# Optimization experiments

Measured on AMD Instinct MI355X. Metric: run time of the kernel, lower is better.

Reference implementation:

```python
import jax, jax.numpy as jnp
import numpy as np

EMBED = 1024
HEADS = 16
HEAD_DIM = EMBED // HEADS          # 64
POS_DIM = 256
POS_PER_HEAD = POS_DIM // HEADS    # 16
POS_IDX = 64
N, L = 8, 1024


def setup_inputs() -> dict:
    key = jax.random.key(0)
    ks = jax.random.split(key, 10)
    s = 0.02
    return {
        "values": jax.random.normal(ks[0], (N, L, EMBED), jnp.float32),
        "keys": jax.random.normal(ks[1], (N, L, EMBED), jnp.float32),
        "query": jax.random.normal(ks[2], (N, L, EMBED), jnp.float32),
        "position": jax.random.normal(ks[3], (N, L, POS_IDX), jnp.float32),
        # torch Linear weights: shape (out_features, in_features)
        "Wv": jax.random.normal(ks[4], (HEAD_DIM, HEAD_DIM), jnp.float32) * s,
        "Wk": jax.random.normal(ks[5], (HEAD_DIM, HEAD_DIM), jnp.float32) * s,
        "Wq": jax.random.normal(ks[6], (HEAD_DIM, HEAD_DIM + POS_PER_HEAD), jnp.float32) * s,
        "Wpos": jax.random.normal(ks[7], (POS_DIM, POS_IDX), jnp.float32) * s,
        "Wo": jax.random.normal(ks[8], (EMBED, EMBED), jnp.float32) * s,
        "bo": jax.random.normal(ks[9], (EMBED,), jnp.float32) * s,
    }


def reference(values, keys, query, position, Wv, Wk, Wq, Wpos, Wo, bo):
    n, qlen = query.shape[0], query.shape[1]
    vlen, klen = values.shape[1], keys.shape[1]
    # position embedding: Linear(pos_idx -> pos_dim)
    pos_emb = position @ Wpos.T                                   # [N, q, POS_DIM]
    q_with_pos = jnp.concatenate([query, pos_emb], axis=2)        # [N, q, EMBED+POS_DIM]
    # split heads
    v = values.reshape(n, vlen, HEADS, HEAD_DIM)
    k = keys.reshape(n, klen, HEADS, HEAD_DIM)
    qp = q_with_pos.reshape(n, qlen, HEADS, HEAD_DIM + POS_PER_HEAD)
    # per-head linear projections (no bias)
    v = jnp.einsum('nlhd,ed->nlhe', v, Wv)
    k = jnp.einsum('nlhd,ed->nlhe', k, Wk)
    q = jnp.einsum('nqhd,ed->nqhe', qp, Wq)
    # attention: note scale uses sqrt(embed_size), as in the original
    energy = jnp.einsum('nqhd,nkhd->nhqk', q, k)
    attn = jax.nn.softmax(energy / jnp.sqrt(jnp.asarray(EMBED, energy.dtype)), axis=3)
    out = jnp.einsum('nhql,nlhd->nqhd', attn, v).reshape(n, qlen, EMBED)
    return out @ Wo.T + bo
```

## Files before the change

### kernel.cpp

```cpp
#include <hip/hip_runtime.h>
#include <hip/hip_bf16.h>


typedef __hip_bfloat16 bf16;
typedef unsigned int u32;
typedef unsigned short u16;
typedef short short8 __attribute__((ext_vector_type(8)));
typedef float f32x4 __attribute__((ext_vector_type(4)));
typedef float f32x16 __attribute__((ext_vector_type(16)));
typedef unsigned int u32x2 __attribute__((ext_vector_type(2)));

#define MFMA16(a, b, c) __builtin_amdgcn_mfma_f32_16x16x32_bf16((a), (b), (c), 0, 0, 0)
#define MFMA32(a, b, c) __builtin_amdgcn_mfma_f32_32x32x16_bf16((a), (b), (c), 0, 0, 0)

#define QSCALE 0.04508422002777998f

__device__ __forceinline__ short8 ld8(const bf16* p) { return *(const short8*)p; }

__device__ __forceinline__ u32 pk2(float a, float b) {
  u16 ua = __bfloat16_as_ushort(__float2bfloat16(a));
  u16 ub = __bfloat16_as_ushort(__float2bfloat16(b));
  return (u32)ua | ((u32)ub << 16);
}

__device__ __forceinline__ float fexp2(float x) {
  float r;
  asm("v_exp_f32 %0, %1" : "=v"(r) : "v"(x));
  return r;
}

__device__ __forceinline__ u32 cvtpk(float a, float b) {
  u32 r;
  asm("v_cvt_pk_bf16_f32 %0, %1, %2" : "=v"(r) : "v"(a), "v"(b));
  return r;
}

__device__ __forceinline__ void gload16(const void* g, void* l) {
  __builtin_amdgcn_global_load_lds(
      (const __attribute__((address_space(1))) u32*)g,
      (__attribute__((address_space(3))) u32*)l, 16, 0, 0);
}

union S8U { short8 s; u32 u[4]; };

__device__ __forceinline__ short8 ld8f(const float* p) {
  float4 a = ((const float4*)p)[0];
  float4 b = ((const float4*)p)[1];
  S8U r;
  r.u[0] = pk2(a.x, a.y);
  r.u[1] = pk2(a.z, a.w);
  r.u[2] = pk2(b.x, b.y);
  r.u[3] = pk2(b.z, b.w);
  return r.s;
}

__global__ __launch_bounds__(256) void fused_pre(
    const float* __restrict__ position, const float* __restrict__ Wpos,
    const float* __restrict__ keys, const float* __restrict__ Wk,
    const float* __restrict__ values, const float* __restrict__ Wv,
    const float* __restrict__ Wo,
    bf16* __restrict__ posb, bf16* __restrict__ kb, bf16* __restrict__ vT,
    bf16* __restrict__ wo16) {
  __shared__ __align__(16) char arena[33280];
  const int bidg = blockIdx.x;
  const int t = threadIdx.x;
  const int lane = t & 63, wave = t >> 6;
  const int g = lane >> 4, c = lane & 15;
  const int wr = wave >> 1, wc = wave & 1;

  if (bidg < 128) {
    const int px = bidg & 63, py = bidg >> 6;
    const int r0 = px * 128 + wr * 64;
    const int c0 = py * 128 + wc * 64;
    f32x4 acc[4][4];
#pragma unroll
    for (int ai = 0; ai < 4; ++ai)
#pragma unroll
      for (int bi = 0; bi < 4; ++bi) acc[ai][bi] = (f32x4){0.f, 0.f, 0.f, 0.f};
#pragma unroll
    for (int k0 = 0; k0 < 64; k0 += 32) {
      short8 af[4], bfr[4];
#pragma unroll
      for (int ai = 0; ai < 4; ++ai)
        af[ai] = ld8f(position + (size_t)(r0 + ai * 16 + c) * 64 + k0 + 8 * g);
#pragma unroll
      for (int bi = 0; bi < 4; ++bi)
        bfr[bi] = ld8f(Wpos + (size_t)(c0 + bi * 16 + c) * 64 + k0 + 8 * g);
#pragma unroll
      for (int ai = 0; ai < 4; ++ai)
#pragma unroll
        for (int bi = 0; bi < 4; ++bi) acc[ai][bi] = MFMA16(af[ai], bfr[bi], acc[ai][bi]);
    }
#pragma unroll
    for (int bi = 0; bi < 4; ++bi) {
      const int p = c0 + bi * 16 + c;
#pragma unroll
      for (int ai = 0; ai < 4; ++ai) {
#pragma unroll
        for (int i = 0; i < 4; ++i) {
          int row = r0 + ai * 16 + 4 * g + i;
          posb[(size_t)row * 256 + p] = __float2bfloat16(acc[ai][bi][i]);
        }
      }
    }
  } else if (bidg < 2176) {
    const bool is_v = (bidg >= 1152);
    const int id = bidg - (is_v ? 1152 : 128);
    const int bx = id & 63, h = id >> 6;
    const float* src = is_v ? values : keys;
    const float* W = is_v ? Wv : Wk;
    f32x4 acc[4][2];
#pragma unroll
    for (int ai = 0; ai < 4; ++ai)
#pragma unroll
      for (int bi = 0; bi < 2; ++bi) acc[ai][bi] = (f32x4){0.f, 0.f, 0.f, 0.f};
    const int r0 = bx * 128;
    const int c0 = wc * 32;
#pragma unroll
    for (int k0 = 0; k0 < 64; k0 += 32) {
      short8 af[4], bfr[2];
#pragma unroll
      for (int ai = 0; ai < 4; ++ai)
        af[ai] = ld8f(src + (size_t)(r0 + wr * 64 + ai * 16 + c) * 1024 + 64 * h + k0 + 8 * g);
#pragma unroll
      for (int bi = 0; bi < 2; ++bi)
        bfr[bi] = ld8f(W + (size_t)(c0 + bi * 16 + c) * 64 + k0 + 8 * g);
#pragma unroll
      for (int ai = 0; ai < 4; ++ai)
#pragma unroll
        for (int bi = 0; bi < 2; ++bi) acc[ai][bi] = MFMA16(af[ai], bfr[bi], acc[ai][bi]);
    }
    if (!is_v) {
      float (*slds)[65] = (float(*)[65])arena;
#pragma unroll
      for (int bi = 0; bi < 2; ++bi) {
        const int e = c0 + bi * 16 + c;
#pragma unroll
        for (int ai = 0; ai < 4; ++ai) {
#pragma unroll
          for (int i = 0; i < 4; ++i)
            slds[wr * 64 + ai * 16 + 4 * g + i][e] = acc[ai][bi][i];
        }
      }
      __syncthreads();
      const int n = r0 >> 10, lb = r0 & 1023;
      bf16* dstp = kb + ((size_t)(n * 16 + h) * 1024 + lb) * 64;
#pragma unroll
      for (int j = 0; j < 4; ++j) {
        const int id2 = t + j * 256;
        const int ll = id2 >> 3, e0 = (id2 & 7) * 8;
        const float* s = &slds[ll][e0];
        S8U r;
        r.u[0] = pk2(s[0], s[1]);
        r.u[1] = pk2(s[2], s[3]);
        r.u[2] = pk2(s[4], s[5]);
        r.u[3] = pk2(s[6], s[7]);
        *(short8*)(dstp + (size_t)ll * 64 + e0) = r.s;
      }
    } else {
      char* tlds = arena;
#pragma unroll
      for (int bi = 0; bi < 2; ++bi) {
        const int e_loc = c0 + bi * 16 + c;
#pragma unroll
        for (int ai = 0; ai < 4; ++ai) {
          const int l0 = wr * 64 + ai * 16 + 4 * g;
          *(u32*)(tlds + e_loc * 272 + l0 * 2) = pk2(acc[ai][bi][0], acc[ai][bi][1]);
          *(u32*)(tlds + e_loc * 272 + l0 * 2 + 4) = pk2(acc[ai][bi][2], acc[ai][bi][3]);
        }
      }
      __syncthreads();
      const int n = bx >> 3;
      const int lglob0 = (bx & 7) * 128;
      bf16* vbase = vT + ((size_t)(n * 16 + h)) * 64 * 1024;
#pragma unroll
      for (int j = 0; j < 4; ++j) {
        const int id2 = t + j * 256;
        const int e = id2 >> 4, lc = (id2 & 15) * 8;
        *(short8*)(vbase + (size_t)e * 1024 + lglob0 + lc) =
            *(const short8*)(tlds + e * 272 + lc * 2);
      }
    }
  } else {
    const int id = bidg - 2176;
    const int i8 = (id * 256 + t) * 8;
    *(short8*)(wo16 + i8) = ld8f(Wo + i8);
  }
}

__global__ __launch_bounds__(256) void q_gemm(const float* __restrict__ query,
                                              const bf16* __restrict__ posb,
                                              const float* __restrict__ Wq,
                                              bf16* __restrict__ qb) {
  __shared__ float slds[128][65];
  const int t = threadIdx.x;
  const int lane = t & 63, wave = t >> 6;
  const int g = lane >> 4, c = lane & 15;
  const int wr = wave >> 1, wc = wave & 1;
  const int r0 = blockIdx.x * 128;
  const int c0 = wc * 32;
  const int h = blockIdx.y;
  f32x4 acc[4][2];
#pragma unroll
  for (int ai = 0; ai < 4; ++ai)
#pragma unroll
    for (int bi = 0; bi < 2; ++bi) acc[ai][bi] = (f32x4){0.f, 0.f, 0.f, 0.f};
  const short8 z8 = (short8){0, 0, 0, 0, 0, 0, 0, 0};
#pragma unroll
  for (int k0 = 0; k0 < 80; k0 += 32) {
    const bool tail_dead = (k0 == 64) && (g >= 2);
    const int col = 80 * h + k0 + 8 * g;
    short8 af[4], bfr[2];
#pragma unroll
    for (int ai = 0; ai < 4; ++ai) {
      const int row = r0 + wr * 64 + ai * 16 + c;
      af[ai] = tail_dead ? z8
               : (col < 1024 ? ld8f(query + (size_t)row * 1024 + col)
                             : ld8(posb + (size_t)row * 256 + (col - 1024)));
    }
#pragma unroll
    for (int bi = 0; bi < 2; ++bi)
      bfr[bi] = tail_dead ? z8
                          : ld8f(Wq + (size_t)(c0 + bi * 16 + c) * 80 + k0 + 8 * g);
#pragma unroll
    for (int ai = 0; ai < 4; ++ai)
#pragma unroll
      for (int bi = 0; bi < 2; ++bi) acc[ai][bi] = MFMA16(af[ai], bfr[bi], acc[ai][bi]);
  }
#pragma unroll
  for (int bi = 0; bi < 2; ++bi) {
    const int e = c0 + bi * 16 + c;
#pragma unroll
    for (int ai = 0; ai < 4; ++ai) {
#pragma unroll
      for (int i = 0; i < 4; ++i)
        slds[wr * 64 + ai * 16 + 4 * g + i][e] = acc[ai][bi][i] * QSCALE;
    }
  }
  __syncthreads();
  const int n = r0 >> 10, lb = r0 & 1023;
  bf16* dstp = qb + ((size_t)(n * 16 + h) * 1024 + lb) * 64;
#pragma unroll
  for (int j = 0; j < 4; ++j) {
    const int id = t + j * 256;
    const int ll = id >> 3, e0 = (id & 7) * 8;
    const float* s = &slds[ll][e0];
    S8U r;
    r.u[0] = pk2(s[0], s[1]);
    r.u[1] = pk2(s[2], s[3]);
    r.u[2] = pk2(s[4], s[5]);
    r.u[3] = pk2(s[6], s[7]);
    *(short8*)(dstp + (size_t)ll * 64 + e0) = r.s;
  }
}

__global__ __launch_bounds__(256, 2) void attn_kernel(const bf16* __restrict__ qb,
                                                      const bf16* __restrict__ kb,
                                                      const bf16* __restrict__ vT,
                                                      bf16* __restrict__ ob) {
  __shared__ __align__(16) char smem[2][16384];
  const int t = threadIdx.x;
  const int lane = t & 63, wave = t >> 6;
  const int l31 = lane & 31, hi = lane >> 5;
  const int bid = blockIdx.x;
  const int w = (bid & 7) * 64 + (bid >> 3);
  const int qt = w & 3, h = (w >> 2) & 15, n = w >> 6;
  const int nh = n * 16 + h;
  const int q0 = qt * 256 + wave * 64;

  const bf16* kpan = kb + (size_t)nh * 65536;
  const bf16* vpan = vT + (size_t)nh * 65536;

  const int sr8 = lane >> 3;
  const int scg = (lane & 7) ^ sr8;
  const int row0 = wave * 8 + sr8;
  const bf16* kgA = kpan + (size_t)row0 * 64 + scg * 8;
  const bf16* kgB = kpan + (size_t)(32 + row0) * 64 + scg * 8;
  const bf16* vgA = vpan + (size_t)row0 * 1024 + scg * 8;
  const bf16* vgB = vpan + (size_t)(32 + row0) * 1024 + scg * 8;
  const int ldsoff = wave * 1024;

  const bf16* qrowA = qb + ((size_t)nh * 1024 + q0 + l31) * 64 + 8 * hi;
  const bf16* qrowB = qrowA + 32 * 64;
  short8 qfA[4], qfB[4];
#pragma unroll
  for (int ds = 0; ds < 4; ++ds) {
    qfA[ds] = ld8(qrowA + ds * 16);
    qfB[ds] = ld8(qrowB + ds * 16);
  }

  f32x16 accA0, accA1, accB0, accB1;
#pragma unroll
  for (int r = 0; r < 16; ++r) {
    accA0[r] = 0.f;
    accA1[r] = 0.f;
    accB0[r] = 0.f;
    accB1[r] = 0.f;
  }
  float lA = 0.f, lB = 0.f;

  gload16(kgA, smem[0] + ldsoff);
  gload16(kgB, smem[0] + 4096 + ldsoff);
  gload16(vgA, smem[0] + 8192 + ldsoff);
  gload16(vgB, smem[0] + 12288 + ldsoff);
  __syncthreads();

  int cur = 0;
  for (int kt = 0; kt < 16; ++kt) {
    if (kt < 15) {
      char* sn = smem[cur ^ 1];
      const size_t ko = (size_t)(kt + 1) * 4096;
      const int vo = (kt + 1) * 64;
      gload16(kgA + ko, sn + ldsoff);
      gload16(kgB + ko, sn + 4096 + ldsoff);
      gload16(vgA + vo, sn + 8192 + ldsoff);
      gload16(vgB + vo, sn + 12288 + ldsoff);
    }
    const char* kt_ = smem[cur];
    const char* vt_ = smem[cur] + 8192;

#pragma unroll
    for (int s = 0; s < 2; ++s) {
      const int kr = s * 32 + l31;
      short8 kf[4], vf[2][2];
#pragma unroll
      for (int ds = 0; ds < 4; ++ds)
        kf[ds] = *(const short8*)(kt_ + kr * 128 + (((2 * ds + hi) ^ (kr & 7)) << 4));
#pragma unroll
      for (int dt = 0; dt < 2; ++dt) {
        const int vr = dt * 32 + l31;
#pragma unroll
        for (int ks = 0; ks < 2; ++ks)
          vf[dt][ks] = *(const short8*)(
              vt_ + vr * 128 + (((s * 4 + ks * 2 + hi) ^ (vr & 7)) << 4));
      }

      f32x16 srA, srB;
#pragma unroll
      for (int r = 0; r < 16; ++r) {
        srA[r] = 0.f;
        srB[r] = 0.f;
      }
      __builtin_amdgcn_s_setprio(1);
      srA = MFMA32(kf[0], qfA[0], srA);
      srA = MFMA32(kf[1], qfA[1], srA);
      srA = MFMA32(kf[2], qfA[2], srA);
      srA = MFMA32(kf[3], qfA[3], srA);
      srB = MFMA32(kf[0], qfB[0], srB);
      srB = MFMA32(kf[1], qfB[1], srB);
      srB = MFMA32(kf[2], qfB[2], srB);
      srB = MFMA32(kf[3], qfB[3], srB);
      __builtin_amdgcn_s_setprio(0);

      float pA[16], pB[16];
#pragma unroll
      for (int r = 0; r < 16; ++r) pA[r] = fexp2(srA[r]);
#pragma unroll
      for (int r = 0; r < 16; ++r) pB[r] = fexp2(srB[r]);

      u32 a01 = cvtpk(pA[0], pA[1]), a23 = cvtpk(pA[2], pA[3]);
      u32 a45 = cvtpk(pA[4], pA[5]), a67 = cvtpk(pA[6], pA[7]);
      u32 a89 = cvtpk(pA[8], pA[9]), aab = cvtpk(pA[10], pA[11]);
      u32 acd = cvtpk(pA[12], pA[13]), aef = cvtpk(pA[14], pA[15]);
      u32x2 sa0 = __builtin_amdgcn_permlane32_swap(a01, a45, false, false);
      u32x2 sa1 = __builtin_amdgcn_permlane32_swap(a23, a67, false, false);
      u32x2 sa2 = __builtin_amdgcn_permlane32_swap(a89, acd, false, false);
      u32x2 sa3 = __builtin_amdgcn_permlane32_swap(aab, aef, false, false);
      S8U pfA0, pfA1;
      pfA0.u[0] = sa0[0];
      pfA0.u[1] = sa1[0];
      pfA0.u[2] = sa0[1];
      pfA0.u[3] = sa1[1];
      pfA1.u[0] = sa2[0];
      pfA1.u[1] = sa3[0];
      pfA1.u[2] = sa2[1];
      pfA1.u[3] = sa3[1];

      u32 b01 = cvtpk(pB[0], pB[1]), b23 = cvtpk(pB[2], pB[3]);
      u32 b45 = cvtpk(pB[4], pB[5]), b67 = cvtpk(pB[6], pB[7]);
      u32 b89 = cvtpk(pB[8], pB[9]), bab = cvtpk(pB[10], pB[11]);
      u32 bcd = cvtpk(pB[12], pB[13]), bef = cvtpk(pB[14], pB[15]);
      u32x2 sb0 = __builtin_amdgcn_permlane32_swap(b01, b45, false, false);
      u32x2 sb1 = __builtin_amdgcn_permlane32_swap(b23, b67, false, false);
      u32x2 sb2 = __builtin_amdgcn_permlane32_swap(b89, bcd, false, false);
      u32x2 sb3 = __builtin_amdgcn_permlane32_swap(bab, bef, false, false);
      S8U pfB0, pfB1;
      pfB0.u[0] = sb0[0];
      pfB0.u[1] = sb1[0];
      pfB0.u[2] = sb0[1];
      pfB0.u[3] = sb1[1];
      pfB1.u[0] = sb2[0];
      pfB1.u[1] = sb3[0];
      pfB1.u[2] = sb2[1];
      pfB1.u[3] = sb3[1];

      __builtin_amdgcn_s_setprio(1);
      accA0 = MFMA32(vf[0][0], pfA0.s, accA0);
      accA0 = MFMA32(vf[0][1], pfA1.s, accA0);
      accA1 = MFMA32(vf[1][0], pfA0.s, accA1);
      accA1 = MFMA32(vf[1][1], pfA1.s, accA1);
      accB0 = MFMA32(vf[0][0], pfB0.s, accB0);
      accB0 = MFMA32(vf[0][1], pfB1.s, accB0);
      accB1 = MFMA32(vf[1][0], pfB0.s, accB1);
      accB1 = MFMA32(vf[1][1], pfB1.s, accB1);
      __builtin_amdgcn_s_setprio(0);

      float psA = ((pA[0] + pA[1]) + (pA[2] + pA[3])) +
                  ((pA[4] + pA[5]) + (pA[6] + pA[7])) +
                  ((pA[8] + pA[9]) + (pA[10] + pA[11])) +
                  ((pA[12] + pA[13]) + (pA[14] + pA[15]));
      float psB = ((pB[0] + pB[1]) + (pB[2] + pB[3])) +
                  ((pB[4] + pB[5]) + (pB[6] + pB[7])) +
                  ((pB[8] + pB[9]) + (pB[10] + pB[11])) +
                  ((pB[12] + pB[13]) + (pB[14] + pB[15]));
      psA += __shfl_xor(psA, 32);
      psB += __shfl_xor(psB, 32);
      lA += psA;
      lB += psB;
    }
    __syncthreads();
    cur ^= 1;
  }

  const float invA = 1.f / lA, invB = 1.f / lB;
  bf16* obaseA = ob + ((size_t)(n * 1024 + q0 + l31) * 16 + h) * 64;
  bf16* obaseB = obaseA + (size_t)32 * 16 * 64;
#pragma unroll
  for (int dt = 0; dt < 2; ++dt) {
#pragma unroll
    for (int rb = 0; rb < 4; ++rb) {
      const int d0 = dt * 32 + rb * 8 + 4 * hi;
      const f32x16& aA = dt ? accA1 : accA0;
      const f32x16& aB = dt ? accB1 : accB0;
      u32x2 wA, wB;
      wA[0] = pk2(aA[4 * rb + 0] * invA, aA[4 * rb + 1] * invA);
      wA[1] = pk2(aA[4 * rb + 2] * invA, aA[4 * rb + 3] * invA);
      wB[0] = pk2(aB[4 * rb + 0] * invB, aB[4 * rb + 1] * invB);
      wB[1] = pk2(aB[4 * rb + 2] * invB, aB[4 * rb + 3] * invB);
      *(u32x2*)(obaseA + d0) = wA;
      *(u32x2*)(obaseB + d0) = wB;
    }
  }
}

__global__ __launch_bounds__(256) void out_gemm(const bf16* __restrict__ A,
                                                const bf16* __restrict__ B,
                                                const float* __restrict__ bias,
                                                float* __restrict__ out) {
  __shared__ __align__(16) char smem[2][32768];
  const int t = threadIdx.x;
  const int lane = t & 63, wave = t >> 6;
  const int g = lane >> 4, c = lane & 15;
  const int wr = wave >> 1, wc = wave & 1;
  const int bid = blockIdx.x;
  const int w = (bid & 7) * 64 + (bid >> 3);
  const int r0 = (w >> 3) * 128;
  const int c0 = (w & 7) * 128;

  const int sr8 = lane >> 3;
  const int scg = (lane & 7) ^ sr8;
  const int row0 = wave * 8 + sr8;
  const bf16* ag = A + (size_t)(r0 + row0) * 1024 + scg * 8;
  const bf16* bg = B + (size_t)(c0 + row0) * 1024 + scg * 8;
  const int ldsoff = wave * 1024;

  f32x4 acc[4][4];
#pragma unroll
  for (int ai = 0; ai < 4; ++ai)
#pragma unroll
    for (int bi = 0; bi < 4; ++bi) acc[ai][bi] = (f32x4){0.f, 0.f, 0.f, 0.f};

#pragma unroll
  for (int j = 0; j < 4; ++j) {
    gload16(ag + (size_t)j * 32 * 1024, smem[0] + j * 4096 + ldsoff);
    gload16(bg + (size_t)j * 32 * 1024, smem[0] + 16384 + j * 4096 + ldsoff);
  }
  __syncthreads();

  int cur = 0;
  for (int kt = 0; kt < 16; ++kt) {
    if (kt < 15) {
      char* sn = smem[cur ^ 1];
      const int k1 = (kt + 1) * 64;
#pragma unroll
      for (int j = 0; j < 4; ++j) {
        gload16(ag + (size_t)j * 32 * 1024 + k1, sn + j * 4096 + ldsoff);
        gload16(bg + (size_t)j * 32 * 1024 + k1, sn + 16384 + j * 4096 + ldsoff);
      }
    }
    const char* sa = smem[cur];
    const char* sb = smem[cur] + 16384;

#pragma unroll
    for (int h2 = 0; h2 < 2; ++h2) {
      short8 af[4], bfr[4];
#pragma unroll
      for (int ai = 0; ai < 4; ++ai) {
        const int row = wr * 64 + ai * 16 + c;
        af[ai] = *(const short8*)(sa + row * 128 + (((h2 * 4 + g) ^ (row & 7)) << 4));
      }
#pragma unroll
      for (int bi = 0; bi < 4; ++bi) {
        const int row = wc * 64 + bi * 16 + c;
        bfr[bi] = *(const short8*)(sb + row * 128 + (((h2 * 4 + g) ^ (row & 7)) << 4));
      }
      __builtin_amdgcn_s_setprio(1);
#pragma unroll
      for (int ai = 0; ai < 4; ++ai)
#pragma unroll
        for (int bi = 0; bi < 4; ++bi) acc[ai][bi] = MFMA16(af[ai], bfr[bi], acc[ai][bi]);
      __builtin_amdgcn_s_setprio(0);
    }

    __syncthreads();
    cur ^= 1;
  }

#pragma unroll
  for (int bi = 0; bi < 4; ++bi) {
    const int e = c0 + wc * 64 + bi * 16 + c;
    const float bv = bias[e];
#pragma unroll
    for (int ai = 0; ai < 4; ++ai) {
#pragma unroll
      for (int i = 0; i < 4; ++i) {
        out[(size_t)(r0 + wr * 64 + ai * 16 + 4 * g + i) * 1024 + e] =
            acc[ai][bi][i] + bv;
      }
    }
  }
}

extern "C" void kernel_launch(void* const* d_in, const int* in_sizes, int n_in,
                              void* d_out, int out_size, void* d_ws, size_t ws_size,
                              hipStream_t stream) {
  const float* values = (const float*)d_in[0];
  const float* keys = (const float*)d_in[1];
  const float* query = (const float*)d_in[2];
  const float* position = (const float*)d_in[3];
  const float* Wv = (const float*)d_in[4];
  const float* Wk = (const float*)d_in[5];
  const float* Wq = (const float*)d_in[6];
  const float* Wpos = (const float*)d_in[7];
  const float* Wo = (const float*)d_in[8];
  const float* bo = (const float*)d_in[9];

  char* ws = (char*)d_ws;
  bf16* qb = (bf16*)(ws);
  bf16* kb = (bf16*)(ws + ((size_t)16 << 20));
  bf16* vT = (bf16*)(ws + ((size_t)32 << 20));
  bf16* posb = (bf16*)(ws + ((size_t)48 << 20));
  bf16* ob = (bf16*)(ws + ((size_t)52 << 20));
  bf16* wo16 = (bf16*)(ws + ((size_t)68 << 20));
  float* out = (float*)d_out;

  fused_pre<<<2688, 256, 0, stream>>>(position, Wpos, keys, Wk, values, Wv, Wo,
                                      posb, kb, vT, wo16);
  q_gemm<<<dim3(64, 16), 256, 0, stream>>>(query, posb, Wq, qb);
  attn_kernel<<<512, 256, 0, stream>>>(qb, kb, vT, ob);
  out_gemm<<<512, 256, 0, stream>>>(ob, wo16, bo, out);
}
```

Baseline: 113.5 us.

## Triple-buffer K/V tiles in attention kernel with single barrier per iteration

The attention kernel's K/V LDS staging moves from double to triple buffering, prefetching two tiles ahead. Explicit vmcnt waits and one raw s_barrier per iteration replace the trailing __syncthreads, which should hide more global-load latency and remove one barrier. The cost is 48KB of LDS per block instead of 32KB, which may limit occupancy under the 2-blocks-per-CU launch bound. Correctness relies on the hand-counted vmcnt(4) matching the four loads issued per stage.

```diff
diff --git a/kernel.cpp b/kernel.cpp
--- a/kernel.cpp
+++ b/kernel.cpp
@@ -258,7 +258,7 @@
                                                       const bf16* __restrict__ kb,
                                                       const bf16* __restrict__ vT,
                                                       bf16* __restrict__ ob) {
-  __shared__ __align__(16) char smem[2][16384];
+  __shared__ __align__(16) char smem[3][16384];
   const int t = threadIdx.x;
   const int lane = t & 63, wave = t >> 6;
   const int l31 = lane & 31, hi = lane >> 5;
@@ -299,23 +299,34 @@
   }
   float lA = 0.f, lB = 0.f;
 
-  gload16(kgA, smem[0] + ldsoff);
-  gload16(kgB, smem[0] + 4096 + ldsoff);
-  gload16(vgA, smem[0] + 8192 + ldsoff);
-  gload16(vgB, smem[0] + 12288 + ldsoff);
-  __syncthreads();
+#define STAGE(sb, kt)                                   \
+  do {                                                  \
+    char* s_ = (sb);                                    \
+    gload16(kgA + (size_t)(kt) * 4096, s_ + ldsoff);    \
+    gload16(kgB + (size_t)(kt) * 4096, s_ + 4096 + ldsoff); \
+    gload16(vgA + (kt) * 64, s_ + 8192 + ldsoff);       \
+    gload16(vgB + (kt) * 64, s_ + 12288 + ldsoff);      \
+  } while (0)
+
+  STAGE(smem[0], 0);
+  STAGE(smem[1], 1);
 
   int cur = 0;
   for (int kt = 0; kt < 16; ++kt) {
-    if (kt < 15) {
-      char* sn = smem[cur ^ 1];
-      const size_t ko = (size_t)(kt + 1) * 4096;
-      const int vo = (kt + 1) * 64;
-      gload16(kgA + ko, sn + ldsoff);
-      gload16(kgB + ko, sn + 4096 + ldsoff);
-      gload16(vgA + vo, sn + 8192 + ldsoff);
-      gload16(vgB + vo, sn + 12288 + ldsoff);
-    }
+    if (kt < 15)
+      asm volatile("s_waitcnt vmcnt(4) lgkmcnt(0)" ::: "memory");
+    else
+      asm volatile("s_waitcnt vmcnt(0) lgkmcnt(0)" ::: "memory");
+    __builtin_amdgcn_sched_barrier(0);
+    __builtin_amdgcn_s_barrier();
+    __builtin_amdgcn_sched_barrier(0);
+    if (kt + 2 < 16) {
+      int nb = cur + 2;
+      if (nb >= 3) nb -= 3;
+      STAGE(smem[nb], kt + 2);
+    }
+    __builtin_amdgcn_sched_barrier(0);
+
     const char* kt_ = smem[cur];
     const char* vt_ = smem[cur] + 8192;
 
@@ -418,9 +429,9 @@
       lA += psA;
       lB += psB;
     }
-    __syncthreads();
-    cur ^= 1;
-  }
+    cur = (cur == 2) ? 0 : cur + 1;
+  }
+#undef STAGE
 
   const float invA = 1.f / lA, invB = 1.f / lB;
   bf16* obaseA = ob + ((size_t)(n * 1024 + q0 + l31) * 16 + h) * 64;
```

After: 114.4 us. Within noise of the previous version (+0.8%).

## Move position-independent Q projection heads into the fused pre-processing kernel

Applied to the files above, without the earlier changes.

Q-projection blocks for heads 0-11 read only query columns, so they do not depend on the position embedding. They are moved into the first fused kernel as extra blocks. The remaining heads 12-15, which need posb, run in a smaller follow-up kernel. This shrinks the serialized second launch and lets the independent Q work overlap with the K/V/pos conversion, at the cost of a larger first grid and a dependency on correct head partitioning.

```diff
diff --git a/kernel.cpp b/kernel.cpp
--- a/kernel.cpp
+++ b/kernel.cpp
@@ -58,9 +58,10 @@
     const float* __restrict__ position, const float* __restrict__ Wpos,
     const float* __restrict__ keys, const float* __restrict__ Wk,
     const float* __restrict__ values, const float* __restrict__ Wv,
-    const float* __restrict__ Wo,
+    const float* __restrict__ Wo, const float* __restrict__ query,
+    const float* __restrict__ Wq,
     bf16* __restrict__ posb, bf16* __restrict__ kb, bf16* __restrict__ vT,
-    bf16* __restrict__ wo16) {
+    bf16* __restrict__ wo16, bf16* __restrict__ qb) {
   __shared__ __align__(16) char arena[33280];
   const int bidg = blockIdx.x;
   const int t = threadIdx.x;
@@ -181,14 +182,70 @@
             *(const short8*)(tlds + e * 272 + lc * 2);
       }
     }
-  } else {
+  } else if (bidg < 2688) {
     const int id = bidg - 2176;
     const int i8 = (id * 256 + t) * 8;
     *(short8*)(wo16 + i8) = ld8f(Wo + i8);
-  }
-}
-
-__global__ __launch_bounds__(256) void q_gemm(const float* __restrict__ query,
+  } else {
+    const int id = bidg - 2688;
+    const int bx = id & 63, h = id >> 6;
+    const int r0 = bx * 128;
+    const int c0 = wc * 32;
+    f32x4 acc[4][2];
+#pragma unroll
+    for (int ai = 0; ai < 4; ++ai)
+#pragma unroll
+      for (int bi = 0; bi < 2; ++bi) acc[ai][bi] = (f32x4){0.f, 0.f, 0.f, 0.f};
+    const short8 z8 = (short8){0, 0, 0, 0, 0, 0, 0, 0};
+#pragma unroll
+    for (int k0 = 0; k0 < 80; k0 += 32) {
+      const bool tail_dead = (k0 == 64) && (g >= 2);
+      const int col = 80 * h + k0 + 8 * g;
+      short8 af[4], bfr[2];
+#pragma unroll
+      for (int ai = 0; ai < 4; ++ai) {
+        const int row = r0 + wr * 64 + ai * 16 + c;
+        af[ai] = tail_dead ? z8 : ld8f(query + (size_t)row * 1024 + col);
+      }
+#pragma unroll
+      for (int bi = 0; bi < 2; ++bi)
+        bfr[bi] = tail_dead ? z8
+                            : ld8f(Wq + (size_t)(c0 + bi * 16 + c) * 80 + k0 + 8 * g);
+#pragma unroll
+      for (int ai = 0; ai < 4; ++ai)
+#pragma unroll
+        for (int bi = 0; bi < 2; ++bi) acc[ai][bi] = MFMA16(af[ai], bfr[bi], acc[ai][bi]);
+    }
+    float (*slds)[65] = (float(*)[65])arena;
+#pragma unroll
+    for (int bi = 0; bi < 2; ++bi) {
+      const int e = c0 + bi * 16 + c;
+#pragma unroll
+      for (int ai = 0; ai < 4; ++ai) {
+#pragma unroll
+        for (int i = 0; i < 4; ++i)
+          slds[wr * 64 + ai * 16 + 4 * g + i][e] = acc[ai][bi][i] * QSCALE;
+      }
+    }
+    __syncthreads();
+    const int n = r0 >> 10, lb = r0 & 1023;
+    bf16* dstp = qb + ((size_t)(n * 16 + h) * 1024 + lb) * 64;
+#pragma unroll
+    for (int j = 0; j < 4; ++j) {
+      const int id2 = t + j * 256;
+      const int ll = id2 >> 3, e0 = (id2 & 7) * 8;
+      const float* s = &slds[ll][e0];
+      S8U r;
+      r.u[0] = pk2(s[0], s[1]);
+      r.u[1] = pk2(s[2], s[3]);
+      r.u[2] = pk2(s[4], s[5]);
+      r.u[3] = pk2(s[6], s[7]);
+      *(short8*)(dstp + (size_t)ll * 64 + e0) = r.s;
+    }
+  }
+}
+
+__global__ __launch_bounds__(256) void q_rest(const float* __restrict__ query,
                                               const bf16* __restrict__ posb,
                                               const float* __restrict__ Wq,
                                               bf16* __restrict__ qb) {
@@ -199,7 +256,7 @@
   const int wr = wave >> 1, wc = wave & 1;
   const int r0 = blockIdx.x * 128;
   const int c0 = wc * 32;
-  const int h = blockIdx.y;
+  const int h = blockIdx.y + 12;
   f32x4 acc[4][2];
 #pragma unroll
   for (int ai = 0; ai < 4; ++ai)
@@ -554,9 +611,9 @@
   bf16* wo16 = (bf16*)(ws + ((size_t)68 << 20));
   float* out = (float*)d_out;
 
-  fused_pre<<<2688, 256, 0, stream>>>(position, Wpos, keys, Wk, values, Wv, Wo,
-                                      posb, kb, vT, wo16);
-  q_gemm<<<dim3(64, 16), 256, 0, stream>>>(query, posb, Wq, qb);
+  fused_pre<<<3456, 256, 0, stream>>>(position, Wpos, keys, Wk, values, Wv, Wo,
+                                      query, Wq, posb, kb, vT, wo16, qb);
+  q_rest<<<dim3(64, 4), 256, 0, stream>>>(query, posb, Wq, qb);
   attn_kernel<<<512, 256, 0, stream>>>(qb, kb, vT, ob);
   out_gemm<<<512, 256, 0, stream>>>(ob, wo16, bo, out);
 }
```

New measurement: 117.2 us. +3.3%, slower.
